# Optimization experiments

Hardware: AMD Instinct MI355X
Metric: run time of the kernel (lower is better)

The kernel has to match this reference:

```python
import jax, jax.numpy as jnp
import numpy as np

RES = (256, 256, 256)
CH = 16
RR = 8  # ceil(log2(256))
N_PTS = 262144


def grid_sample_2d(plane, gx, gy):
    """Bilinear grid_sample, align_corners=True.
    plane: (C, H, W); gx in [-1,1] indexes W, gy indexes H. Returns (N, C)."""
    C, H, W = plane.shape
    ix = (gx + 1.0) * 0.5 * (W - 1)
    iy = (gy + 1.0) * 0.5 * (H - 1)
    x0f = jnp.floor(ix)
    y0f = jnp.floor(iy)
    wx = ix - x0f
    wy = iy - y0f
    x0 = jnp.clip(x0f.astype(jnp.int32), 0, W - 1)
    x1 = jnp.clip(x0 + 1, 0, W - 1)
    y0 = jnp.clip(y0f.astype(jnp.int32), 0, H - 1)
    y1 = jnp.clip(y0 + 1, 0, H - 1)
    v00 = plane[:, y0, x0]  # (C, N)
    v01 = plane[:, y0, x1]
    v10 = plane[:, y1, x0]
    v11 = plane[:, y1, x1]
    out = (v00 * (1 - wx) * (1 - wy) + v01 * wx * (1 - wy)
           + v10 * (1 - wx) * wy + v11 * wx * wy)
    return out.T  # (N, C)


def integrate(P, coords):
    """P: (N, 2*CH, RR) with real part channels [:CH], imag [CH:].
    coords: (N,) in [-1,1]. Fourier-basis numerical integration (real part)."""
    c = (coords + 1.0) * 0.5 * (2 ** RR - 1)  # (N,)
    coef = jnp.concatenate([jnp.zeros((1,), jnp.float32),
                            2.0 ** jnp.arange(RR - 1, dtype=jnp.float32)]) / (2 ** RR)
    theta = 2.0 * jnp.pi * c[:, None] * coef  # (N, RR)
    # Re(exp(i*theta) . P_complex) = cos.Re(P) - sin.Im(P)
    re = jnp.einsum('nr,ncr->nc', jnp.cos(theta), P[:, :CH, :])
    im = jnp.einsum('nr,ncr->nc', jnp.sin(theta), P[:, CH:, :])
    return re - im  # (N, CH)


def setup_inputs() -> dict:
    key = jax.random.key(0)
    k0, k1, k2, k3 = jax.random.split(key, 4)
    inputs = jax.random.uniform(k0, (N_PTS, 3), dtype=jnp.float32,
                                minval=-1.0, maxval=1.0)
    C = 2 * RR * CH
    Pu = 0.001 * jax.random.normal(k1, (1, C, RES[1], RES[2]), dtype=jnp.float32)
    Pv = 0.001 * jax.random.normal(k2, (1, C, RES[0], RES[2]), dtype=jnp.float32)
    Pw = 0.001 * jax.random.normal(k3, (1, C, RES[0], RES[1]), dtype=jnp.float32)
    return {"inputs": inputs, "Pu": Pu, "Pv": Pv, "Pw": Pw}


def reference(inputs, Pu, Pv, Pw):
    c0, c1, c2 = inputs[:, 0], inputs[:, 1], inputs[:, 2]
    # grid last-dim (x,y): x indexes width (last plane axis), y the height.
    su = grid_sample_2d(Pu[0], c1, c2).reshape(-1, 2 * CH, RR)
    sv = grid_sample_2d(Pv[0], c0, c2).reshape(-1, 2 * CH, RR)
    sw = grid_sample_2d(Pw[0], c0, c1).reshape(-1, 2 * CH, RR)
    return integrate(su, c0) + integrate(sv, c1) + integrate(sw, c2)  # (N, CH)
```

## Files before the change

### kernel.cpp

```cpp
#include <hip/hip_runtime.h>
#include <hip/hip_fp16.h>
#include <math.h>

#define NPTS 262144
#define PLANE_ELEMS 16777216u

typedef __attribute__((ext_vector_type(4))) float f4;
typedef __attribute__((ext_vector_type(4))) unsigned int u4;

#define OFF_IDX      (3ull * PLANE_ELEMS * 2ull)
#define OFF_PARTIAL  (OFF_IDX + (size_t)3 * NPTS * 4)
#define OFF_HIST     (OFF_PARTIAL + (size_t)2 * NPTS * 16 * 2)
#define WS_NEED      (OFF_HIST + (size_t)3 * 65536 * 4)

__device__ __forceinline__ void plane_xy(int p, float c0, float c1, float c2,
                                         float& gx, float& gy, float& ax) {
  if (p == 0)      { gx = c1; gy = c2; ax = c0; }
  else if (p == 1) { gx = c0; gy = c2; ax = c1; }
  else             { gx = c0; gy = c1; ax = c2; }
}

__device__ __forceinline__ int cell_of(float g) {
  float i = (g + 1.f) * 0.5f * 255.f;
  int x0 = (int)floorf(i);
  return x0 < 0 ? 0 : (x0 > 255 ? 255 : x0);
}

__device__ __forceinline__ void trans_load(const float* __restrict__ src,
                                           unsigned c0, unsigned hw0, int tid,
                                           f4 (&va)[4], f4 (&vb)[4]) {
#pragma unroll
  for (int j = 0; j < 4; ++j) {
    int idx = j * 256 + tid;
    int rp = idx >> 5;
    int q = idx & 31;
    const f4* base = (const f4*)(src + (size_t)(c0 + 2 * rp) * 65536u + hw0 + 4 * q);
    va[j] = __builtin_nontemporal_load(base);
    vb[j] = __builtin_nontemporal_load(base + 16384);
  }
}

__device__ __forceinline__ void trans_proc(unsigned* tile, __half* dst,
                                           unsigned c0, unsigned hw0, int tid,
                                           f4 (&va)[4], f4 (&vb)[4]) {
#pragma unroll
  for (int j = 0; j < 4; ++j) {
    int idx = j * 256 + tid;
    int rp = idx >> 5;
    int q = idx & 31;
#pragma unroll
    for (int k = 0; k < 4; ++k) {
      int hw = 4 * q + k;
      __half2 h = __floats2half2_rn(va[j][k], vb[j][k]);
      tile[hw * 36 + (rp ^ (hw >> 3))] = *(unsigned*)&h;
    }
  }
  __syncthreads();
  int seg = tid & 7;
#pragma unroll
  for (int jj = 0; jj < 4; ++jj) {
    int hw = jj * 32 + (tid >> 3);
    int s = hw >> 3;
    u4 v = *(const u4*)(tile + hw * 36 + 4 * ((seg ^ (s >> 2)) & 7));
    u4 o;
    switch (s & 3) {
      case 0: o = v; break;
      case 1: o = u4{v.y, v.x, v.w, v.z}; break;
      case 2: o = u4{v.z, v.w, v.x, v.y}; break;
      default: o = u4{v.w, v.z, v.y, v.x}; break;
    }
    *(u4*)((char*)dst + ((size_t)(hw0 + hw) * 256u + c0) * 2u + seg * 16u) = o;
  }
  __syncthreads();
}

template <int FINAL>
__device__ __forceinline__ void samp_point(
    int p, int slot, int t, const unsigned* __restrict__ idx,
    const float* __restrict__ inputs, const __half* __restrict__ T,
    __half* __restrict__ partial, float* __restrict__ out) {
  unsigned n = idx[(size_t)p * NPTS + slot];
  float c0 = inputs[n * 3 + 0], c1 = inputs[n * 3 + 1], c2 = inputs[n * 3 + 2];
  float gx, gy, ax;
  plane_xy(p, c0, c1, c2, gx, gy, ax);

  float ix = (gx + 1.f) * 0.5f * 255.f;
  float iy = (gy + 1.f) * 0.5f * 255.f;
  float x0f = floorf(ix), y0f = floorf(iy);
  float wx = ix - x0f, wy = iy - y0f;
  int x0 = (int)x0f; x0 = x0 < 0 ? 0 : (x0 > 255 ? 255 : x0);
  int y0 = (int)y0f; y0 = y0 < 0 ? 0 : (y0 > 255 ? 255 : y0);
  int x1 = x0 + 1 > 255 ? 255 : x0 + 1;
  int y1 = y0 + 1 > 255 ? 255 : y0 + 1;
  float w00 = (1.f - wx) * (1.f - wy);
  float w01 = wx * (1.f - wy);
  float w10 = (1.f - wx) * wy;
  float w11 = wx * wy;

  const __half* __restrict__ P = T + (size_t)p * PLANE_ELEMS;
  int r00 = (y0 * 256 + x0) * 256, r01 = (y0 * 256 + x1) * 256;
  int r10 = (y1 * 256 + x0) * 256, r11 = (y1 * 256 + x1) * 256;
  int ore = t * 16;
  int oim = 128 + t * 16;

  f4 a0 = *(const f4*)(P + r00 + ore),     a1 = *(const f4*)(P + r00 + ore + 8);
  f4 a2 = *(const f4*)(P + r00 + oim),     a3 = *(const f4*)(P + r00 + oim + 8);
  f4 b0 = *(const f4*)(P + r01 + ore),     b1 = *(const f4*)(P + r01 + ore + 8);
  f4 b2 = *(const f4*)(P + r01 + oim),     b3 = *(const f4*)(P + r01 + oim + 8);
  f4 c0v = *(const f4*)(P + r10 + ore),    c1v = *(const f4*)(P + r10 + ore + 8);
  f4 c2v = *(const f4*)(P + r10 + oim),    c3v = *(const f4*)(P + r10 + oim + 8);
  f4 d0 = *(const f4*)(P + r11 + ore),     d1 = *(const f4*)(P + r11 + ore + 8);
  f4 d2 = *(const f4*)(P + r11 + oim),     d3 = *(const f4*)(P + r11 + oim + 8);

  __half2 hw00 = __float2half2_rn(w00), hw01 = __float2half2_rn(w01);
  __half2 hw10 = __float2half2_rn(w10), hw11 = __float2half2_rn(w11);

  __half2 bre[8], bim[8];
#pragma unroll
  for (int q = 0; q < 4; ++q) {
    __half2 v;
    v = __hmul2(((const __half2*)&a0)[q], hw00);
    v = __hfma2(((const __half2*)&b0)[q],  hw01, v);
    v = __hfma2(((const __half2*)&c0v)[q], hw10, v);
    bre[q] = __hfma2(((const __half2*)&d0)[q], hw11, v);

    v = __hmul2(((const __half2*)&a1)[q], hw00);
    v = __hfma2(((const __half2*)&b1)[q],  hw01, v);
    v = __hfma2(((const __half2*)&c1v)[q], hw10, v);
    bre[q + 4] = __hfma2(((const __half2*)&d1)[q], hw11, v);

    v = __hmul2(((const __half2*)&a2)[q], hw00);
    v = __hfma2(((const __half2*)&b2)[q],  hw01, v);
    v = __hfma2(((const __half2*)&c2v)[q], hw10, v);
    bim[q] = __hfma2(((const __half2*)&d2)[q], hw11, v);

    v = __hmul2(((const __half2*)&a3)[q], hw00);
    v = __hfma2(((const __half2*)&b3)[q],  hw01, v);
    v = __hfma2(((const __half2*)&c3v)[q], hw10, v);
    bim[q + 4] = __hfma2(((const __half2*)&d3)[q], hw11, v);
  }

  float fre[16], fim[16];
#pragma unroll
  for (int q = 0; q < 8; ++q) {
    float2 vr = __half22float2(bre[q]);
    float2 vi = __half22float2(bim[q]);
    fre[2 * q] = vr.x; fre[2 * q + 1] = vr.y;
    fim[2 * q] = vi.x; fim[2 * q + 1] = vi.y;
  }

  float cs = (ax + 1.f) * 0.5f * 255.f;
  float th = 6.283185307179586f * cs * (1.f / 256.f);
  float s, c;
  __sincosf(th, &s, &c);
  float aR0 = fre[0], aR1 = fre[8];
  float aI0 = 0.f,    aI1 = 0.f;
#pragma unroll
  for (int r = 1; r < 8; ++r) {
    aR0 += fre[r] * c;     aR1 += fre[8 + r] * c;
    aI0 += fim[r] * s;     aI1 += fim[8 + r] * s;
    if (r < 7) {
      float c2 = c + c;
      float cn = c2 * c - 1.f;
      s = c2 * s;
      c = cn;
    }
  }

  if (FINAL) {
    const size_t PS = (size_t)NPTS * 16;
    float2 p0 = __half22float2(*(const __half2*)(partial + (size_t)n * 16 + 2 * t));
    float2 p1 = __half22float2(*(const __half2*)(partial + PS + (size_t)n * 16 + 2 * t));
    float2 o;
    o.x = (aR0 - aI0) + p0.x + p1.x;
    o.y = (aR1 - aI1) + p0.y + p1.y;
    *(float2*)(out + (size_t)n * 16 + 2 * t) = o;
  } else {
    *(__half2*)(partial + ((size_t)p * NPTS + n) * 16 + 2 * t) =
        __floats2half2_rn(aR0 - aI0, aR1 - aI1);
  }
}

__device__ __forceinline__ void scat_point(
    int p, int n, const float* __restrict__ inputs,
    unsigned* __restrict__ hist, unsigned* __restrict__ idx) {
  float c0 = inputs[n * 3 + 0], c1 = inputs[n * 3 + 1], c2 = inputs[n * 3 + 2];
  float gx, gy, ax;
  plane_xy(p, c0, c1, c2, gx, gy, ax);
  int key = (cell_of(gy) << 8) | cell_of(gx);
  unsigned pos = atomicAdd(&hist[p * 65536 + key], 1u);
  idx[(size_t)p * NPTS + pos] = (unsigned)n;
}

__global__ __launch_bounds__(256) void PREFFFT_fat1_k(
    const float* __restrict__ Pu, const float* __restrict__ Pv,
    const float* __restrict__ Pw, __half* __restrict__ dst0,
    const float* __restrict__ inputs, unsigned* __restrict__ hist) {
  __shared__ unsigned tile[128 * 36];
  const int bx = blockIdx.x;
  const int tid = threadIdx.x;
  if ((bx % 3) != 2) {
    int ti = (bx / 3) * 2 + (bx % 3);
    int bz = ti / 512;
    int rem = ti - bz * 512;
    int by = rem >> 7;
    int bxx = rem & 127;
    const float* src = bz == 0 ? Pu : (bz == 1 ? Pv : Pw);
    __half* dst = dst0 + (size_t)bz * PLANE_ELEMS;
    const unsigned hwbase = bxx * 512u;
    const unsigned c0 = by * 64u;
    f4 vaA[4], vbA[4], vaB[4], vbB[4];
    trans_load(src, c0, hwbase, tid, vaA, vbA);
    trans_load(src, c0, hwbase + 128u, tid, vaB, vbB);
    trans_proc(tile, dst, c0, hwbase, tid, vaA, vbA);
    trans_load(src, c0, hwbase + 256u, tid, vaA, vbA);
    trans_proc(tile, dst, c0, hwbase + 128u, tid, vaB, vbB);
    trans_load(src, c0, hwbase + 384u, tid, vaB, vbB);
    trans_proc(tile, dst, c0, hwbase + 256u, tid, vaA, vbA);
    trans_proc(tile, dst, c0, hwbase + 384u, tid, vaB, vbB);
  } else {
    int hb = bx / 3;
#pragma unroll
    for (int it = 0; it < 4; ++it) {
      int item = hb * 1024 + it * 256 + tid;
      int n = item & (NPTS - 1);
      int p = item >> 18;
      float c0 = inputs[n * 3 + 0], c1 = inputs[n * 3 + 1], c2 = inputs[n * 3 + 2];
      float gx, gy, ax;
      plane_xy(p, c0, c1, c2, gx, gy, ax);
      int key = (cell_of(gy) << 8) | cell_of(gx);
      atomicAdd(&hist[p * 65536 + key], 1u);
    }
  }
}

__global__ __launch_bounds__(1024) void PREFFFT_scan_k(unsigned* __restrict__ hist) {
  __shared__ unsigned part[1024];
  unsigned* h = hist + (size_t)blockIdx.x * 65536;
  int t = threadIdx.x;
  unsigned s = 0;
#pragma unroll 8
  for (int i = 0; i < 64; ++i) s += h[t * 64 + i];
  part[t] = s;
  __syncthreads();
  for (int off = 1; off < 1024; off <<= 1) {
    unsigned v = (t >= off) ? part[t - off] : 0u;
    __syncthreads();
    part[t] += v;
    __syncthreads();
  }
  unsigned run = (t == 0) ? 0u : part[t - 1];
#pragma unroll 8
  for (int i = 0; i < 64; ++i) {
    unsigned c = h[t * 64 + i];
    h[t * 64 + i] = run;
    run += c;
  }
}

__global__ __launch_bounds__(256) void PREFFFT_scat1_k(
    const float* __restrict__ inputs, unsigned* __restrict__ hist,
    unsigned* __restrict__ idx) {
  int n = blockIdx.x * 256 + threadIdx.x;
  scat_point(0, n, inputs, hist, idx);
}

__global__ __launch_bounds__(256) void PREFFFT_fat2_k(
    unsigned* __restrict__ idx, const float* __restrict__ inputs,
    const __half* __restrict__ T, __half* __restrict__ partial,
    unsigned* __restrict__ hist, int sp) {
  int bx = blockIdx.x;
  if (bx < 1024) {
    int n = bx * 256 + threadIdx.x;
    scat_point(sp + 1, n, inputs, hist, idx);
  } else {
    int b = bx - 1024;
    int lbx = (b & 7) * 1024 + (b >> 3);
    int slot = lbx * 32 + ((int)threadIdx.x >> 3);
    samp_point<0>(sp, slot, threadIdx.x & 7, idx, inputs, T, partial, nullptr);
  }
}

__global__ __launch_bounds__(256) void PREFFFT_samp2out_k(
    const unsigned* __restrict__ idx, const float* __restrict__ inputs,
    const __half* __restrict__ T, __half* __restrict__ partial,
    float* __restrict__ out) {
  int b = blockIdx.x;
  int lbx = (b & 7) * 1024 + (b >> 3);
  int slot = lbx * 32 + ((int)threadIdx.x >> 3);
  samp_point<1>(2, slot, threadIdx.x & 7, idx, inputs, T, partial, out);
}

__global__ __launch_bounds__(256) void PREFFFT_fallback_k(
    const float* __restrict__ inputs, const float* __restrict__ Tu,
    const float* __restrict__ Tv, const float* __restrict__ Tw,
    float* __restrict__ out) {
  int gtid = blockIdx.x * 256 + threadIdx.x;
  int n = gtid >> 5;
  int t = threadIdx.x & 31;
  const bool is_re = t < 16;
  float c0 = inputs[n * 3 + 0], c1 = inputs[n * 3 + 1], c2 = inputs[n * 3 + 2];
  const float* PL[3] = {Tu, Tv, Tw};
  float acc = 0.f;
#pragma unroll
  for (int p = 0; p < 3; ++p) {
    float gx, gy, ax;
    plane_xy(p, c0, c1, c2, gx, gy, ax);
    float ix = (gx + 1.f) * 0.5f * 255.f;
    float iy = (gy + 1.f) * 0.5f * 255.f;
    float x0f = floorf(ix), y0f = floorf(iy);
    float wx = ix - x0f, wy = iy - y0f;
    int x0 = (int)x0f; x0 = x0 < 0 ? 0 : (x0 > 255 ? 255 : x0);
    int y0 = (int)y0f; y0 = y0 < 0 ? 0 : (y0 > 255 ? 255 : y0);
    int x1 = x0 + 1 > 255 ? 255 : x0 + 1;
    int y1 = y0 + 1 > 255 ? 255 : y0 + 1;
    float w00 = (1.f - wx) * (1.f - wy), w01 = wx * (1.f - wy);
    float w10 = (1.f - wx) * wy, w11 = wx * wy;
    int i00 = y0 * 256 + x0, i01 = y0 * 256 + x1;
    int i10 = y1 * 256 + x0, i11 = y1 * 256 + x1;
    float b[8];
#pragma unroll
    for (int j = 0; j < 8; ++j) {
      const float* base = PL[p] + (size_t)(t * 8 + j) * 65536u;
      b[j] = w00 * base[i00] + w01 * base[i01] + w10 * base[i10] + w11 * base[i11];
    }
    float csv = (ax + 1.f) * 0.5f * 255.f;
    float theta1 = 6.283185307179586f * csv * (1.f / 256.f);
    float partial = is_re ? b[0] : 0.f;
#pragma unroll
    for (int r = 1; r < 8; ++r) {
      float thr = theta1 * (float)(1 << (r - 1));
      float s, c;
      __sincosf(thr, &s, &c);
      partial += b[r] * (is_re ? c : s);
    }
    float other = __shfl_xor(partial, 16);
    acc += partial - other;
  }
  if (is_re) out[n * 16 + t] = acc;
}

extern "C" void kernel_launch(void* const* d_in, const int* in_sizes, int n_in,
                              void* d_out, int out_size, void* d_ws, size_t ws_size,
                              hipStream_t stream) {
  const float* inputs = (const float*)d_in[0];
  const float* Pu = (const float*)d_in[1];
  const float* Pv = (const float*)d_in[2];
  const float* Pw = (const float*)d_in[3];
  float* out = (float*)d_out;

  if (ws_size >= WS_NEED) {
    char* ws = (char*)d_ws;
    __half*   T       = (__half*)ws;
    unsigned* idx     = (unsigned*)(ws + OFF_IDX);
    __half*   partial = (__half*)(ws + OFF_PARTIAL);
    unsigned* hist    = (unsigned*)(ws + OFF_HIST);

    hipMemsetAsync(hist, 0, (size_t)3 * 65536 * 4, stream);
    PREFFFT_fat1_k<<<2304, 256, 0, stream>>>(Pu, Pv, Pw, T, inputs, hist);
    PREFFFT_scan_k<<<3, 1024, 0, stream>>>(hist);
    PREFFFT_scat1_k<<<1024, 256, 0, stream>>>(inputs, hist, idx);
    PREFFFT_fat2_k<<<9216, 256, 0, stream>>>(idx, inputs, T, partial, hist, 0);
    PREFFFT_fat2_k<<<9216, 256, 0, stream>>>(idx, inputs, T, partial, hist, 1);
    PREFFFT_samp2out_k<<<8192, 256, 0, stream>>>(idx, inputs, T, partial, out);
  } else {
    PREFFFT_fallback_k<<<NPTS / 8, 256, 0, stream>>>(inputs, Pu, Pv, Pw, out);
  }
}
```

Measured before the change: 195.0 us.

## Split fused transpose/histogram kernel to overlap plane-0 scatter with remaining transposes

The fused transpose+histogram kernel is split in two. The first transposes plane Pu and builds only the plane-0 histogram, then a single-block scan runs. The second kernel transposes Pv and Pw, builds the plane-1 and plane-2 histograms, and runs the plane-0 scatter alongside them, followed by a two-block scan. This removes the standalone scatter launch and hides scatter work behind transpose bandwidth, at the cost of an extra scan launch and a serialized first phase.

```diff
diff --git a/kernel.cpp b/kernel.cpp
--- a/kernel.cpp
+++ b/kernel.cpp
@@ -72,6 +72,41 @@
     *(u4*)((char*)dst + ((size_t)(hw0 + hw) * 256u + c0) * 2u + seg * 16u) = o;
   }
   __syncthreads();
+}
+
+__device__ __forceinline__ void trans_unit(const float* __restrict__ src,
+                                           __half* __restrict__ dst,
+                                           unsigned hwbase, unsigned c0, int tid,
+                                           unsigned* tile) {
+  f4 vaA[4], vbA[4], vaB[4], vbB[4];
+  trans_load(src, c0, hwbase, tid, vaA, vbA);
+  trans_load(src, c0, hwbase + 128u, tid, vaB, vbB);
+  trans_proc(tile, dst, c0, hwbase, tid, vaA, vbA);
+  trans_load(src, c0, hwbase + 256u, tid, vaA, vbA);
+  trans_proc(tile, dst, c0, hwbase + 128u, tid, vaB, vbB);
+  trans_load(src, c0, hwbase + 384u, tid, vaB, vbB);
+  trans_proc(tile, dst, c0, hwbase + 256u, tid, vaA, vbA);
+  trans_proc(tile, dst, c0, hwbase + 384u, tid, vaB, vbB);
+}
+
+__device__ __forceinline__ void hist_point(
+    int p, int n, const float* __restrict__ inputs, unsigned* __restrict__ hist) {
+  float c0 = inputs[n * 3 + 0], c1 = inputs[n * 3 + 1], c2 = inputs[n * 3 + 2];
+  float gx, gy, ax;
+  plane_xy(p, c0, c1, c2, gx, gy, ax);
+  int key = (cell_of(gy) << 8) | cell_of(gx);
+  atomicAdd(&hist[p * 65536 + key], 1u);
+}
+
+__device__ __forceinline__ void scat_point(
+    int p, int n, const float* __restrict__ inputs,
+    unsigned* __restrict__ hist, unsigned* __restrict__ idx) {
+  float c0 = inputs[n * 3 + 0], c1 = inputs[n * 3 + 1], c2 = inputs[n * 3 + 2];
+  float gx, gy, ax;
+  plane_xy(p, c0, c1, c2, gx, gy, ax);
+  int key = (cell_of(gy) << 8) | cell_of(gx);
+  unsigned pos = atomicAdd(&hist[p * 65536 + key], 1u);
+  idx[(size_t)p * NPTS + pos] = (unsigned)n;
 }
 
 template <int FINAL>
@@ -181,62 +216,64 @@
   }
 }
 
-__device__ __forceinline__ void scat_point(
-    int p, int n, const float* __restrict__ inputs,
-    unsigned* __restrict__ hist, unsigned* __restrict__ idx) {
-  float c0 = inputs[n * 3 + 0], c1 = inputs[n * 3 + 1], c2 = inputs[n * 3 + 2];
-  float gx, gy, ax;
-  plane_xy(p, c0, c1, c2, gx, gy, ax);
-  int key = (cell_of(gy) << 8) | cell_of(gx);
-  unsigned pos = atomicAdd(&hist[p * 65536 + key], 1u);
-  idx[(size_t)p * NPTS + pos] = (unsigned)n;
-}
-
-__global__ __launch_bounds__(256) void PREFFFT_fat1_k(
-    const float* __restrict__ Pu, const float* __restrict__ Pv,
-    const float* __restrict__ Pw, __half* __restrict__ dst0,
+__global__ __launch_bounds__(256) void PREFFFT_fat1a_k(
+    const float* __restrict__ Pu, __half* __restrict__ dst0,
     const float* __restrict__ inputs, unsigned* __restrict__ hist) {
   __shared__ unsigned tile[128 * 36];
   const int bx = blockIdx.x;
   const int tid = threadIdx.x;
   if ((bx % 3) != 2) {
     int ti = (bx / 3) * 2 + (bx % 3);
-    int bz = ti / 512;
-    int rem = ti - bz * 512;
+    int by = ti >> 7;
+    int bxx = ti & 127;
+    trans_unit(Pu, dst0, bxx * 512u, by * 64u, tid, tile);
+  } else {
+    int hb = bx / 3;
+#pragma unroll
+    for (int it = 0; it < 4; ++it) {
+      int n = hb * 1024 + it * 256 + tid;
+      hist_point(0, n, inputs, hist);
+    }
+  }
+}
+
+__global__ __launch_bounds__(256) void PREFFFT_fat1b_k(
+    const float* __restrict__ Pv, const float* __restrict__ Pw,
+    __half* __restrict__ dst0, const float* __restrict__ inputs,
+    unsigned* __restrict__ hist, unsigned* __restrict__ idx) {
+  __shared__ unsigned tile[128 * 36];
+  const int bx = blockIdx.x;
+  const int tid = threadIdx.x;
+  int r = bx % 5, q5 = bx / 5;
+  if (r < 2) {
+    int u = q5 * 2 + r;
+    int bz = 1 + (u >> 9);
+    int rem = u & 511;
     int by = rem >> 7;
     int bxx = rem & 127;
-    const float* src = bz == 0 ? Pu : (bz == 1 ? Pv : Pw);
-    __half* dst = dst0 + (size_t)bz * PLANE_ELEMS;
-    const unsigned hwbase = bxx * 512u;
-    const unsigned c0 = by * 64u;
-    f4 vaA[4], vbA[4], vaB[4], vbB[4];
-    trans_load(src, c0, hwbase, tid, vaA, vbA);
-    trans_load(src, c0, hwbase + 128u, tid, vaB, vbB);
-    trans_proc(tile, dst, c0, hwbase, tid, vaA, vbA);
-    trans_load(src, c0, hwbase + 256u, tid, vaA, vbA);
-    trans_proc(tile, dst, c0, hwbase + 128u, tid, vaB, vbB);
-    trans_load(src, c0, hwbase + 384u, tid, vaB, vbB);
-    trans_proc(tile, dst, c0, hwbase + 256u, tid, vaA, vbA);
-    trans_proc(tile, dst, c0, hwbase + 384u, tid, vaB, vbB);
-  } else {
-    int hb = bx / 3;
+    const float* src = bz == 1 ? Pv : Pw;
+    trans_unit(src, dst0 + (size_t)bz * PLANE_ELEMS, bxx * 512u, by * 64u,
+               tid, tile);
+  } else if (r == 2) {
+    int hb = q5;
 #pragma unroll
     for (int it = 0; it < 4; ++it) {
       int item = hb * 1024 + it * 256 + tid;
       int n = item & (NPTS - 1);
-      int p = item >> 18;
-      float c0 = inputs[n * 3 + 0], c1 = inputs[n * 3 + 1], c2 = inputs[n * 3 + 2];
-      float gx, gy, ax;
-      plane_xy(p, c0, c1, c2, gx, gy, ax);
-      int key = (cell_of(gy) << 8) | cell_of(gx);
-      atomicAdd(&hist[p * 65536 + key], 1u);
-    }
-  }
-}
-
-__global__ __launch_bounds__(1024) void PREFFFT_scan_k(unsigned* __restrict__ hist) {
+      int p = 1 + (item >> 18);
+      hist_point(p, n, inputs, hist);
+    }
+  } else {
+    int sb = q5 * 2 + (r - 3);
+    int n = sb * 256 + tid;
+    scat_point(0, n, inputs, hist, idx);
+  }
+}
+
+__global__ __launch_bounds__(1024) void PREFFFT_scan_k(unsigned* __restrict__ hist,
+                                                       int pbase) {
   __shared__ unsigned part[1024];
-  unsigned* h = hist + (size_t)blockIdx.x * 65536;
+  unsigned* h = hist + (size_t)(pbase + blockIdx.x) * 65536;
   int t = threadIdx.x;
   unsigned s = 0;
 #pragma unroll 8
@@ -256,13 +293,6 @@
     h[t * 64 + i] = run;
     run += c;
   }
-}
-
-__global__ __launch_bounds__(256) void PREFFFT_scat1_k(
-    const float* __restrict__ inputs, unsigned* __restrict__ hist,
-    unsigned* __restrict__ idx) {
-  int n = blockIdx.x * 256 + threadIdx.x;
-  scat_point(0, n, inputs, hist, idx);
 }
 
 __global__ __launch_bounds__(256) void PREFFFT_fat2_k(
@@ -357,9 +387,10 @@
     unsigned* hist    = (unsigned*)(ws + OFF_HIST);
 
     hipMemsetAsync(hist, 0, (size_t)3 * 65536 * 4, stream);
-    PREFFFT_fat1_k<<<2304, 256, 0, stream>>>(Pu, Pv, Pw, T, inputs, hist);
-    PREFFFT_scan_k<<<3, 1024, 0, stream>>>(hist);
-    PREFFFT_scat1_k<<<1024, 256, 0, stream>>>(inputs, hist, idx);
+    PREFFFT_fat1a_k<<<768, 256, 0, stream>>>(Pu, T, inputs, hist);
+    PREFFFT_scan_k<<<1, 1024, 0, stream>>>(hist, 0);
+    PREFFFT_fat1b_k<<<2560, 256, 0, stream>>>(Pv, Pw, T, inputs, hist, idx);
+    PREFFFT_scan_k<<<2, 1024, 0, stream>>>(hist, 1);
     PREFFFT_fat2_k<<<9216, 256, 0, stream>>>(idx, inputs, T, partial, hist, 0);
     PREFFFT_fat2_k<<<9216, 256, 0, stream>>>(idx, inputs, T, partial, hist, 1);
     PREFFFT_samp2out_k<<<8192, 256, 0, stream>>>(idx, inputs, T, partial, out);
```

After: 224.3 us. +15.0%, slower.
